# Kernel tuning notes

Measured on AMD Instinct MI355X. Metric: run time of the kernel, lower is better.

## Reference

```python
import jax, jax.numpy as jnp
import numpy as np

ALPHA = 0.2        # LeakyReLU negative slope
K_NUM = 16         # top-k kept per row
NEG_INF = -9e15    # mask fill value from original code


def setup_inputs() -> dict:
    key = jax.random.key(0)
    k1, k2, k3, k4 = jax.random.split(key, 4)
    B, N, F_in, F_out = 4, 2048, 512, 512
    h = jax.random.normal(k1, (B, N, F_in), dtype=jnp.float32)
    adj = jax.random.randint(k2, (B, N, N), 0, 2, dtype=jnp.int32)
    # xavier_uniform with gain=1.414
    def xavier(k, shape, gain=1.414):
        fan_in, fan_out = shape[0], shape[1]
        bound = gain * np.sqrt(6.0 / (fan_in + fan_out))
        return jax.random.uniform(k, shape, jnp.float32, -bound, bound)
    W = xavier(k3, (F_in, F_out))
    a = xavier(k4, (2 * F_out, 1))
    return {"h": h, "adj": adj, "W": W, "a": a}


def reference(h, adj, W, a):
    # h: [B,N,F_in], adj: [B,N,N], W: [F_in,F_out], a: [2*F_out,1]
    F_out = W.shape[1]
    Wh = jnp.einsum('bnf,fo->bno', h, W)                       # [B,N,F_out]
    # concat-attention trick: e[b,i,j] = leaky(Wh_i . a1 + Wh_j . a2)
    a1, a2 = a[:F_out, 0], a[F_out:, 0]
    e_src = Wh @ a1                                            # [B,N]
    e_dst = Wh @ a2                                            # [B,N]
    e = e_src[:, :, None] + e_dst[:, None, :]                  # [B,N,N]
    e = jnp.where(e > 0, e, ALPHA * e)                         # LeakyReLU
    e = jnp.where(adj > 0, e, NEG_INF)
    attention = jax.nn.softmax(e, axis=2)                      # [B,N,N]
    # dropout is identity in eval mode (training=False)
    topk_vals = jax.lax.top_k(attention, K_NUM)[0]             # [B,N,K]
    kth = topk_vals[:, :, -1:]                                 # [B,N,1]
    attention = jnp.where(attention < kth, 0.0, attention)
    h_prime = jnp.einsum('bij,bjo->bio', attention, Wh)        # [B,N,F_out]
    return jax.nn.elu(h_prime)                                 # concat=True
```

## Files before the change

### kernel.cpp

```cpp
#include <hip/hip_runtime.h>

typedef unsigned short u16;
typedef short short8 __attribute__((ext_vector_type(8)));
typedef float f32x4 __attribute__((ext_vector_type(4)));

static __device__ __forceinline__ u16 f32_to_bf16(float f) {
  unsigned u = __float_as_uint(f);
  u += 0x7FFFu + ((u >> 16) & 1u);
  return (u16)(u >> 16);
}
static __device__ __forceinline__ float bfLO(unsigned v) { return __uint_as_float(v << 16); }
static __device__ __forceinline__ float bfHI(unsigned v) { return __uint_as_float(v & 0xFFFF0000u); }

static __device__ __forceinline__ void gl_lds16(const void* g, void* l) {
  __builtin_amdgcn_global_load_lds((const __attribute__((address_space(1))) void*)g,
                                   (__attribute__((address_space(3))) void*)l, 16, 0, 0);
}

__global__ __launch_bounds__(256) void k0_prep(const float* __restrict__ W,
                                               const float* __restrict__ a,
                                               u16* __restrict__ Wt,
                                               float* __restrict__ w1,
                                               float* __restrict__ w2) {
  int bid = blockIdx.x;
  int t = threadIdx.x;
  if (bid < 64) {
    __shared__ float tile[64][65];
    int tx = (bid & 7) * 64;
    int ty = (bid >> 3) * 64;
    int rl = t >> 4;
    int cb = (t & 15) * 4;
#pragma unroll
    for (int p = 0; p < 4; ++p) {
      float4 v = *(const float4*)(W + (size_t)(ty + rl + p * 16) * 512 + tx + cb);
      tile[rl + p * 16][cb + 0] = v.x;
      tile[rl + p * 16][cb + 1] = v.y;
      tile[rl + p * 16][cb + 2] = v.z;
      tile[rl + p * 16][cb + 3] = v.w;
    }
    __syncthreads();
#pragma unroll
    for (int p = 0; p < 4; ++p) {
      int n = tx + rl + p * 16;
      ushort4 o;
      o.x = f32_to_bf16(tile[cb + 0][rl + p * 16]);
      o.y = f32_to_bf16(tile[cb + 1][rl + p * 16]);
      o.z = f32_to_bf16(tile[cb + 2][rl + p * 16]);
      o.w = f32_to_bf16(tile[cb + 3][rl + p * 16]);
      *(ushort4*)(Wt + (size_t)n * 512 + ty + cb) = o;
    }
  } else {
    int i = (bid - 64) * 4 + (t >> 6);
    int lane = t & 63;
    const float* row = W + (size_t)i * 512;
    float s1 = 0.f, s2 = 0.f;
#pragma unroll
    for (int q = 0; q < 2; ++q) {
      float4 wv = *(const float4*)(row + lane * 8 + q * 4);
      float4 x1 = *(const float4*)(a + lane * 8 + q * 4);
      float4 x2 = *(const float4*)(a + 512 + lane * 8 + q * 4);
      s1 += wv.x * x1.x + wv.y * x1.y + wv.z * x1.z + wv.w * x1.w;
      s2 += wv.x * x2.x + wv.y * x2.y + wv.z * x2.z + wv.w * x2.w;
    }
#pragma unroll
    for (int d = 32; d; d >>= 1) { s1 += __shfl_xor(s1, d); s2 += __shfl_xor(s2, d); }
    if (lane == 0) { w1[i] = s1; w2[i] = s2; }
  }
}

__global__ __launch_bounds__(256) void k1_rows(const float* __restrict__ h,
                                               const float* __restrict__ w1,
                                               const float* __restrict__ w2,
                                               float* __restrict__ es,
                                               float* __restrict__ ed,
                                               u16* __restrict__ hbf) {
  int r = blockIdx.x * 4 + (threadIdx.x >> 6);
  int lane = threadIdx.x & 63;
  const float* row = h + (size_t)r * 512 + lane * 8;
  float4 v0 = *(const float4*)(row);
  float4 v1 = *(const float4*)(row + 4);
  uint4 pk;
  pk.x = (unsigned)f32_to_bf16(v0.x) | ((unsigned)f32_to_bf16(v0.y) << 16);
  pk.y = (unsigned)f32_to_bf16(v0.z) | ((unsigned)f32_to_bf16(v0.w) << 16);
  pk.z = (unsigned)f32_to_bf16(v1.x) | ((unsigned)f32_to_bf16(v1.y) << 16);
  pk.w = (unsigned)f32_to_bf16(v1.z) | ((unsigned)f32_to_bf16(v1.w) << 16);
  *(uint4*)(hbf + (size_t)r * 512 + lane * 8) = pk;
  float4 x0 = *(const float4*)(w1 + lane * 8);
  float4 x1 = *(const float4*)(w1 + lane * 8 + 4);
  float4 y0 = *(const float4*)(w2 + lane * 8);
  float4 y1 = *(const float4*)(w2 + lane * 8 + 4);
  float s1 = v0.x * x0.x + v0.y * x0.y + v0.z * x0.z + v0.w * x0.w +
             v1.x * x1.x + v1.y * x1.y + v1.z * x1.z + v1.w * x1.w;
  float s2 = v0.x * y0.x + v0.y * y0.y + v0.z * y0.z + v0.w * y0.w +
             v1.x * y1.x + v1.y * y1.y + v1.z * y1.z + v1.w * y1.w;
#pragma unroll
  for (int d = 32; d; d >>= 1) { s1 += __shfl_xor(s1, d); s2 += __shfl_xor(s2, d); }
  if (lane == 0) { es[r] = s1; ed[r] = s2; }
}

__global__ __launch_bounds__(256) void k2_gemm(const u16* __restrict__ hbf,
                                               const u16* __restrict__ Wt,
                                               u16* __restrict__ Whb,
                                               const float* __restrict__ ed,
                                               uint2* __restrict__ edp) {
  __shared__ __align__(16) u16 As[2][128 * 32];
  __shared__ __align__(16) u16 Bs[2][64 * 32];
  int t = threadIdx.x;
  int L = blockIdx.x;

  if (L >= 512) {
    int q = L - 512;
    int bb = q >> 5;
    int seg = q & 31;
    int lane = t & 63, wvv = t >> 6;
    const float* edb = ed + bb * 2048;
    float4 vals[8];
#pragma unroll
    for (int c = 0; c < 8; ++c) vals[c] = *(const float4*)(edb + c * 256 + lane * 4);
    float vk = edb[seg * 64 + wvv * 16 + (lane & 15)];
#pragma unroll 1
    for (int k = 0; k < 16; ++k) {
      int i = seg * 64 + wvv * 16 + k;
      float vi = __shfl(vk, k);
      int rank = 0;
#pragma unroll
      for (int c = 0; c < 8; ++c) {
        int jb = c * 256 + lane * 4;
        rank += (int)(vals[c].x > vi) + (int)((vals[c].x == vi) & (jb + 0 < i));
        rank += (int)(vals[c].y > vi) + (int)((vals[c].y == vi) & (jb + 1 < i));
        rank += (int)(vals[c].z > vi) + (int)((vals[c].z == vi) & (jb + 2 < i));
        rank += (int)(vals[c].w > vi) + (int)((vals[c].w == vi) & (jb + 3 < i));
      }
#pragma unroll
      for (int d = 32; d; d >>= 1) rank += __shfl_xor(rank, d);
      if (lane == 0) edp[bb * 2048 + rank] = make_uint2(__float_as_uint(vi), (unsigned)i);
    }
    return;
  }

  int lane = t & 63;
  int wv = t >> 6;
  int xcd = L & 7, g = L >> 3;
  int m0 = (xcd * 8 + (g >> 3)) * 128;
  int n0 = (g & 7) * 64;
  int wr = (wv >> 1) * 64, wc = (wv & 1) * 32;
  f32x4 zero = {0.f, 0.f, 0.f, 0.f};
  f32x4 acc[4][2];
#pragma unroll
  for (int i = 0; i < 4; ++i)
#pragma unroll
    for (int j = 0; j < 2; ++j) acc[i][j] = zero;
  int kb = (lane >> 4) * 8;
  int mm = lane & 15;
  int sA0 = t, sA1 = t + 256;
  const u16* gA0 = hbf + (size_t)(m0 + (sA0 >> 2)) * 512 + (sA0 & 3) * 8;
  const u16* gA1 = hbf + (size_t)(m0 + (sA1 >> 2)) * 512 + (sA1 & 3) * 8;
  const u16* gB = Wt + (size_t)(n0 + (t >> 2)) * 512 + (t & 3) * 8;

  gl_lds16(gA0, (char*)As[0] + sA0 * 16);
  gl_lds16(gA1, (char*)As[0] + sA1 * 16);
  gl_lds16(gB, (char*)Bs[0] + t * 16);
  __syncthreads();

  for (int step = 0; step < 16; ++step) {
    int cur = step & 1;
    if (step < 15) {
      int kt = (step + 1) * 32;
      gl_lds16(gA0 + kt, (char*)As[cur ^ 1] + sA0 * 16);
      gl_lds16(gA1 + kt, (char*)As[cur ^ 1] + sA1 * 16);
      gl_lds16(gB + kt, (char*)Bs[cur ^ 1] + t * 16);
    }
    short8 af[4], bfr[2];
#pragma unroll
    for (int mi = 0; mi < 4; ++mi)
      af[mi] = *(const short8*)(As[cur] + (wr + mi * 16 + mm) * 32 + kb);
#pragma unroll
    for (int ni = 0; ni < 2; ++ni)
      bfr[ni] = *(const short8*)(Bs[cur] + (wc + ni * 16 + mm) * 32 + kb);
#pragma unroll
    for (int mi = 0; mi < 4; ++mi)
#pragma unroll
      for (int ni = 0; ni < 2; ++ni)
        acc[mi][ni] = __builtin_amdgcn_mfma_f32_16x16x32_bf16(af[mi], bfr[ni], acc[mi][ni], 0, 0, 0);
    __syncthreads();
  }
  int r4 = (lane >> 4) * 4;
  int cc = lane & 15;
#pragma unroll
  for (int mi = 0; mi < 4; ++mi)
#pragma unroll
    for (int ni = 0; ni < 2; ++ni)
#pragma unroll
      for (int rr = 0; rr < 4; ++rr) {
        int grow = m0 + wr + mi * 16 + r4 + rr;
        int gcol = n0 + wc + ni * 16 + cc;
        Whb[(size_t)grow * 512 + gcol] = f32_to_bf16(acc[mi][ni][rr]);
      }
}

__global__ __launch_bounds__(256, 4) void k3_attn(const int* __restrict__ adj,
                                                  const float* __restrict__ es,
                                                  const uint2* __restrict__ edp,
                                                  const float* __restrict__ ed,
                                                  const u16* __restrict__ Whb,
                                                  float* __restrict__ out) {
  __shared__ unsigned vms[4][64];
  __shared__ uint2 lst[4][64];
  int wv = threadIdx.x >> 6, lane = threadIdx.x & 63;
  int L = blockIdx.x;
  int xcd = L & 7, g = L >> 3;
  int r = (xcd >> 1) * 2048 + (xcd & 1) * 1024 + g * 4 + wv;
  int b = r >> 11;
  lst[wv][lane] = make_uint2(0u, 0u);
  float esi = es[r];
  const uint2* edpb = edp + ((size_t)b << 11);
  uint2 cd0 = edpb[lane];
  const int4* arow = (const int4*)(adj + ((size_t)r << 11));
  const float4* edr = (const float4*)(ed + ((size_t)b << 11));

  unsigned vm = 0;
  float ss = 0.f;
#pragma unroll
  for (int t = 0; t < 8; ++t) {
    int4 a4 = arow[t * 64 + lane];
    float4 e4 = edr[t * 64 + lane];
    float ee[4] = {e4.x, e4.y, e4.z, e4.w};
    int aa[4] = {a4.x, a4.y, a4.z, a4.w};
#pragma unroll
    for (int c = 0; c < 4; ++c) {
      float xx = esi + ee[c];
      float el = fmaxf(xx, 0.2f * xx);
      bool valid = aa[c] > 0;
      vm |= (valid ? 1u : 0u) << (t * 4 + c);
      ss += valid ? __expf(el) : 0.f;
    }
  }
  vms[wv][lane] = vm;
#pragma unroll
  for (int d = 32; d; d >>= 1) ss += __shfl_xor(ss, d);

  unsigned long long lmlt = (1ull << lane) - 1ull;
  int cnt = 0;
#define WALK(CD)                                                            \
  {                                                                         \
    float edv = __uint_as_float((CD).x);                                    \
    int j = (int)(CD).y;                                                    \
    unsigned wd = vms[wv][(j >> 2) & 63];                                   \
    bool val = (wd >> (((j >> 8) << 2) | (j & 3))) & 1u;                    \
    unsigned long long mk = __ballot(val);                                  \
    float xx = esi + edv;                                                   \
    float el = fmaxf(xx, 0.2f * xx);                                        \
    float pv = __expf(el);                                                  \
    int rk = cnt + (int)__popcll(mk & lmlt);                                \
    if (val && rk < 64) lst[wv][rk] = make_uint2((CD).y, __float_as_uint(pv)); \
    cnt += (int)__popcll(mk);                                               \
  }
  WALK(cd0)
  for (int c0 = 64; c0 < 2048 && cnt < 20; c0 += 64) {
    uint2 cd = edpb[c0 + lane];
    WALK(cd)
  }
#undef WALK
  if (cnt > 64) cnt = 64;

  const u16* WhB = Whb + ((size_t)b << 20);
  float4 acc0 = {0.f, 0.f, 0.f, 0.f}, acc1 = {0.f, 0.f, 0.f, 0.f};

#define FMA8(U, AV)                                              \
    acc0.x += (AV) * bfLO(U.x); acc0.y += (AV) * bfHI(U.x);      \
    acc0.z += (AV) * bfLO(U.y); acc0.w += (AV) * bfHI(U.y);      \
    acc1.x += (AV) * bfLO(U.z); acc1.y += (AV) * bfHI(U.z);      \
    acc1.z += (AV) * bfLO(U.w); acc1.w += (AV) * bfHI(U.w);

  float pwA[8];
  uint4 uA[8];
#pragma unroll
  for (int t = 0; t < 8; ++t) {
    uint2 lt = lst[wv][t];
    pwA[t] = __uint_as_float(lt.y);
    uA[t] = ((const uint4*)(WhB + ((size_t)lt.x << 9)))[lane];
  }
#pragma unroll
  for (int t = 0; t < 8; ++t) { FMA8(uA[t], pwA[t]) }

  float pwB[8];
  uint4 uB[8];
#pragma unroll
  for (int t = 0; t < 8; ++t) {
    uint2 lt = lst[wv][t + 8];
    pwB[t] = __uint_as_float(lt.y);
    uB[t] = ((const uint4*)(WhB + ((size_t)lt.x << 9)))[lane];
  }
#pragma unroll
  for (int t = 0; t < 8; ++t) { FMA8(uB[t], pwB[t]) }

  float p16v = __uint_as_float(lst[wv][15].y);
  float akq = p16v / ss;
  for (int t2 = 16; t2 < cnt; ++t2) {
    uint2 lt = lst[wv][t2];
    float pvt = __uint_as_float(lt.y);
    if ((pvt / ss) < akq) break;
    uint4 u = ((const uint4*)(WhB + ((size_t)lt.x << 9)))[lane];
    FMA8(u, pvt)
  }
#undef FMA8

  float rss = 1.0f / ss;
  float4 o0, o1;
  o0.x = acc0.x * rss; o0.y = acc0.y * rss; o0.z = acc0.z * rss; o0.w = acc0.w * rss;
  o1.x = acc1.x * rss; o1.y = acc1.y * rss; o1.z = acc1.z * rss; o1.w = acc1.w * rss;
  o0.x = o0.x > 0.f ? o0.x : (__expf(o0.x) - 1.0f);
  o0.y = o0.y > 0.f ? o0.y : (__expf(o0.y) - 1.0f);
  o0.z = o0.z > 0.f ? o0.z : (__expf(o0.z) - 1.0f);
  o0.w = o0.w > 0.f ? o0.w : (__expf(o0.w) - 1.0f);
  o1.x = o1.x > 0.f ? o1.x : (__expf(o1.x) - 1.0f);
  o1.y = o1.y > 0.f ? o1.y : (__expf(o1.y) - 1.0f);
  o1.z = o1.z > 0.f ? o1.z : (__expf(o1.z) - 1.0f);
  o1.w = o1.w > 0.f ? o1.w : (__expf(o1.w) - 1.0f);
  float* ob = out + ((size_t)r << 9) + lane * 8;
  *(float4*)(ob) = o0;
  *(float4*)(ob + 4) = o1;
}

extern "C" void kernel_launch(void* const* d_in, const int* in_sizes, int n_in,
                              void* d_out, int out_size, void* d_ws, size_t ws_size,
                              hipStream_t stream) {
  const float* h = (const float*)d_in[0];
  const int* adj = (const int*)d_in[1];
  const float* W = (const float*)d_in[2];
  const float* a = (const float*)d_in[3];
  float* out = (float*)d_out;
  char* ws = (char*)d_ws;

  u16* Whb = (u16*)(ws);
  u16* hbf = (u16*)(ws + 8388608);
  u16* Wt = (u16*)(ws + 16777216);
  uint2* edp = (uint2*)(ws + 16777216 + 524288);
  float* es = (float*)(ws + 16777216 + 524288 + 65536);
  float* ed = es + 8192;
  float* w1 = ed + 8192;
  float* w2 = w1 + 512;

  hipLaunchKernelGGL(k0_prep, dim3(192), dim3(256), 0, stream, W, a, Wt, w1, w2);
  hipLaunchKernelGGL(k1_rows, dim3(2048), dim3(256), 0, stream, h, w1, w2, es, ed, hbf);
  hipLaunchKernelGGL(k2_gemm, dim3(640), dim3(256), 0, stream, hbf, Wt, Whb, ed, edp);
  hipLaunchKernelGGL(k3_attn, dim3(2048), dim3(256), 0, stream, adj, es, edp, ed, Whb, out);
}
```

Baseline: 51.78 us.

## Move adjacency mask and softmax denominator pass into the GEMM launch

The pass that streams the int32 adjacency rows to build validity bitmasks and softmax row sums moves out of the attention kernel and into extra blocks of the GEMM launch. Those blocks write the masks and sums to workspace, and the attention kernel reads them back. The goal is to overlap the 64 MB adjacency read with the bf16 GEMM. The cost is a 2 MB mask round trip through global memory and a much larger grid for the GEMM kernel, whose extra blocks compete for CUs with the GEMM tiles.

New measurement: 45.41 us (median of 2 runs). -12.3%, faster.

```diff
diff --git a/kernel.cpp b/kernel.cpp
--- a/kernel.cpp
+++ b/kernel.cpp
@@ -102,11 +102,48 @@
                                                const u16* __restrict__ Wt,
                                                u16* __restrict__ Whb,
                                                const float* __restrict__ ed,
-                                               uint2* __restrict__ edp) {
+                                               uint2* __restrict__ edp,
+                                               const int* __restrict__ adj,
+                                               const float* __restrict__ es,
+                                               unsigned* __restrict__ vms_g,
+                                               float* __restrict__ ss_g) {
   __shared__ __align__(16) u16 As[2][128 * 32];
   __shared__ __align__(16) u16 Bs[2][64 * 32];
   int t = threadIdx.x;
   int L = blockIdx.x;
+
+  if (L >= 640) {
+    int q = L - 640;
+    int wv = t >> 6, lane = t & 63;
+    int xcd = q & 7, g = q >> 3;
+    int r = (xcd >> 1) * 2048 + (xcd & 1) * 1024 + g * 4 + wv;
+    int b = r >> 11;
+    float esi = es[r];
+    const int4* arow = (const int4*)(adj + ((size_t)r << 11));
+    const float4* edr = (const float4*)(ed + ((size_t)b << 11));
+    unsigned vm = 0;
+    float ss = 0.f;
+#pragma unroll
+    for (int u = 0; u < 8; ++u) {
+      int4 a4 = arow[u * 64 + lane];
+      float4 e4 = edr[u * 64 + lane];
+      float ee[4] = {e4.x, e4.y, e4.z, e4.w};
+      int aa[4] = {a4.x, a4.y, a4.z, a4.w};
+#pragma unroll
+      for (int c = 0; c < 4; ++c) {
+        float xx = esi + ee[c];
+        float el = fmaxf(xx, 0.2f * xx);
+        bool valid = aa[c] > 0;
+        vm |= (valid ? 1u : 0u) << (u * 4 + c);
+        ss += valid ? __expf(el) : 0.f;
+      }
+    }
+    vms_g[((size_t)r << 6) + lane] = vm;
+#pragma unroll
+    for (int d = 32; d; d >>= 1) ss += __shfl_xor(ss, d);
+    if (lane == 0) ss_g[r] = ss;
+    return;
+  }
 
   if (L >= 512) {
     int q = L - 512;
@@ -198,10 +235,10 @@
       }
 }
 
-__global__ __launch_bounds__(256, 4) void k3_attn(const int* __restrict__ adj,
+__global__ __launch_bounds__(256, 4) void k3_attn(const unsigned* __restrict__ vms_g,
+                                                  const float* __restrict__ ss_g,
                                                   const float* __restrict__ es,
                                                   const uint2* __restrict__ edp,
-                                                  const float* __restrict__ ed,
                                                   const u16* __restrict__ Whb,
                                                   float* __restrict__ out) {
   __shared__ unsigned vms[4][64];
@@ -212,32 +249,11 @@
   int r = (xcd >> 1) * 2048 + (xcd & 1) * 1024 + g * 4 + wv;
   int b = r >> 11;
   lst[wv][lane] = make_uint2(0u, 0u);
+  vms[wv][lane] = vms_g[((size_t)r << 6) + lane];
+  float ss = ss_g[r];
   float esi = es[r];
   const uint2* edpb = edp + ((size_t)b << 11);
   uint2 cd0 = edpb[lane];
-  const int4* arow = (const int4*)(adj + ((size_t)r << 11));
-  const float4* edr = (const float4*)(ed + ((size_t)b << 11));
-
-  unsigned vm = 0;
-  float ss = 0.f;
-#pragma unroll
-  for (int t = 0; t < 8; ++t) {
-    int4 a4 = arow[t * 64 + lane];
-    float4 e4 = edr[t * 64 + lane];
-    float ee[4] = {e4.x, e4.y, e4.z, e4.w};
-    int aa[4] = {a4.x, a4.y, a4.z, a4.w};
-#pragma unroll
-    for (int c = 0; c < 4; ++c) {
-      float xx = esi + ee[c];
-      float el = fmaxf(xx, 0.2f * xx);
-      bool valid = aa[c] > 0;
-      vm |= (valid ? 1u : 0u) << (t * 4 + c);
-      ss += valid ? __expf(el) : 0.f;
-    }
-  }
-  vms[wv][lane] = vm;
-#pragma unroll
-  for (int d = 32; d; d >>= 1) ss += __shfl_xor(ss, d);
 
   unsigned long long lmlt = (1ull << lane) - 1ull;
   int cnt = 0;
@@ -336,13 +352,16 @@
   u16* hbf = (u16*)(ws + 8388608);
   u16* Wt = (u16*)(ws + 16777216);
   uint2* edp = (uint2*)(ws + 16777216 + 524288);
-  float* es = (float*)(ws + 16777216 + 524288 + 65536);
+  unsigned* vms_g = (unsigned*)(ws + 16777216 + 524288 + 65536);
+  float* es = (float*)(ws + 16777216 + 524288 + 65536 + 2097152);
   float* ed = es + 8192;
   float* w1 = ed + 8192;
   float* w2 = w1 + 512;
+  float* ss_g = w2 + 512;
 
   hipLaunchKernelGGL(k0_prep, dim3(192), dim3(256), 0, stream, W, a, Wt, w1, w2);
   hipLaunchKernelGGL(k1_rows, dim3(2048), dim3(256), 0, stream, h, w1, w2, es, ed, hbf);
-  hipLaunchKernelGGL(k2_gemm, dim3(640), dim3(256), 0, stream, hbf, Wt, Whb, ed, edp);
-  hipLaunchKernelGGL(k3_attn, dim3(2048), dim3(256), 0, stream, adj, es, edp, ed, Whb, out);
-}
+  hipLaunchKernelGGL(k2_gemm, dim3(2688), dim3(256), 0, stream, hbf, Wt, Whb, ed, edp,
+                     adj, es, vms_g, ss_g);
+  hipLaunchKernelGGL(k3_attn, dim3(2048), dim3(256), 0, stream, vms_g, ss_g, es, edp, Whb, out);
+}
```
